# Kernel tuning notes

Hardware: AMD Instinct MI355X
Metric: run time of the kernel (lower is better)

The kernel has to match this reference:

```python
import jax, jax.numpy as jnp
import numpy as np

D_K = 64  # key/query head dim used for the 1/sqrt(d_k) scale


def setup_inputs() -> dict:
    key0 = jax.random.key(0)
    kk, kq, kv = jax.random.split(key0, 3)
    B, H, S, DK, DV = 2, 16, 2048, 64, 64
    return {
        "key": jax.random.normal(kk, (B, H, S, DK), dtype=jnp.float32),
        "query": jax.random.normal(kq, (B, H, S, DK), dtype=jnp.float32),
        "value": jax.random.normal(kv, (B, H, S, DV), dtype=jnp.float32),
    }


def reference(key, query, value):
    # scaled dot-product attention per head: [B,H,S,S]
    scores = jnp.einsum("bhqd,bhkd->bhqk", query, key) / jnp.sqrt(jnp.asarray(D_K, query.dtype))
    attn = jax.nn.softmax(scores, axis=-1)
    out = jnp.einsum("bhqk,bhkv->bhqv", attn, value)  # [B,H,S,d_v]
    B, H, S, DV = out.shape
    # faithful to the torch .view: raw reshape (no head transpose)
    return out.reshape(B, S, H * DV)
```

## Files before the change

kernel.cpp:

```cpp
#include <hip/hip_runtime.h>

#define S_LEN 2048
#define DHEAD 64
#define BHEADS 32
#define BM 128
#define BN 64
#define NTILES (S_LEN / BN)
#define HEAD_ELEMS (S_LEN * DHEAD)
#define TENS_ELEMS (BHEADS * HEAD_ELEMS)

typedef _Float16 half8_t __attribute__((ext_vector_type(8)));
typedef _Float16 half4_t __attribute__((ext_vector_type(4)));
typedef _Float16 half2_t __attribute__((ext_vector_type(2)));
typedef float float4_t __attribute__((ext_vector_type(4)));

#define SC_LOG2E 0.18033688011112042f

__device__ __forceinline__ void async_cp16(const void* g, void* l) {
    __builtin_amdgcn_global_load_lds(
        (const __attribute__((address_space(1))) unsigned int*)g,
        (__attribute__((address_space(3))) unsigned int*)l, 16, 0, 0);
}

__global__ void prep_kernel(const float* __restrict__ K,
                            const float* __restrict__ V,
                            _Float16* __restrict__ K16,
                            _Float16* __restrict__ VT) {
    __shared__ _Float16 tile[64][72];
    const int bh = blockIdx.x >> 5;
    const int s0 = (blockIdx.x & 31) * 64;
    const int tid = threadIdx.x;

    const float4* ks = (const float4*)(K + (bh * S_LEN + s0) * DHEAD);
    half4_t* kd = (half4_t*)(K16 + (bh * S_LEN + s0) * DHEAD);
    const float4* vs = (const float4*)(V + (bh * S_LEN + s0) * DHEAD);
#pragma unroll
    for (int it = 0; it < 4; ++it) {
        int i = it * 256 + tid;
        float4 kv = ks[i];
        half4_t h = {(_Float16)(kv.x * SC_LOG2E), (_Float16)(kv.y * SC_LOG2E),
                     (_Float16)(kv.z * SC_LOG2E), (_Float16)(kv.w * SC_LOG2E)};
        kd[i] = h;
        float4 vv = vs[i];
        int r = i >> 4, c4 = (i & 15) * 4;
        half4_t hv = {(_Float16)vv.x, (_Float16)vv.y, (_Float16)vv.z, (_Float16)vv.w};
        *(half4_t*)&tile[r][c4] = hv;
    }
    __syncthreads();
    _Float16* vd = VT + bh * HEAD_ELEMS + s0;
#pragma unroll
    for (int it = 0; it < 2; ++it) {
        int c = it * 256 + tid;
        int vrow = c >> 3, p0 = (c & 7) * 8;
        half8_t h;
#pragma unroll
        for (int j = 0; j < 8; ++j) {
            int p = p0 + j, pc = p >> 2;
            int key = ((pc >> 3) << 5) + ((pc & 1) << 4) + (((pc >> 1) & 3) << 2) + (p & 3);
            h[j] = tile[key][vrow];
        }
        *(half8_t*)(vd + vrow * S_LEN + p0) = h;
    }
}


__global__ __launch_bounds__(256) void attn_kernel(
    const float* __restrict__ Qf,
    const _Float16* __restrict__ K16,
    const _Float16* __restrict__ VT16,
    float* __restrict__ out) {
    __shared__ __align__(16) _Float16 sQ[BM * DHEAD];
    __shared__ __align__(16) _Float16 sK[2][BN * DHEAD];
    __shared__ __align__(16) _Float16 sVT[2][BN * DHEAD];

    const int tid = threadIdx.x;
    const int wave = tid >> 6;
    const int lane = tid & 63;
    const int ln15 = lane & 15;
    const int g = lane >> 4;

    const int bh = blockIdx.x >> 4;
    const int q0 = (blockIdx.x & 15) * BM;

    const float* Qg = Qf + (bh * S_LEN + q0) * DHEAD;
    const _Float16* Kg = K16 + bh * HEAD_ELEMS;
    const _Float16* Vg = VT16 + bh * HEAD_ELEMS;

    const int c0 = tid, c1 = tid + 256;
    const int r0 = c0 >> 3, r1 = c1 >> 3;
    const int sl0 = (c0 - r0) & 7, sl1 = (c1 - r1) & 7;
    const _Float16* ksrc0 = Kg + r0 * DHEAD + sl0 * 8;
    const _Float16* ksrc1 = Kg + r1 * DHEAD + sl1 * 8;
    const _Float16* vsrc0 = Vg + r0 * S_LEN + sl0 * 8;
    const _Float16* vsrc1 = Vg + r1 * S_LEN + sl1 * 8;
    _Float16* kd0[2] = {sK[0] + c0 * 8, sK[1] + c0 * 8};
    _Float16* kd1[2] = {sK[0] + c1 * 8, sK[1] + c1 * 8};
    _Float16* vd0[2] = {sVT[0] + c0 * 8, sVT[1] + c0 * 8};
    _Float16* vd1[2] = {sVT[0] + c1 * 8, sVT[1] + c1 * 8};

    async_cp16(ksrc0, kd0[0]);
    async_cp16(ksrc1, kd1[0]);
    async_cp16(vsrc0, vd0[0]);
    async_cp16(vsrc1, vd1[0]);

#pragma unroll
    for (int tt = 0; tt < 4; ++tt) {
        int c = tid + tt * 256;
        int row = c >> 3;
        int lsl = (c - row) & 7;
        const float4* src = (const float4*)(Qg + row * DHEAD + lsl * 8);
        float4 v0 = src[0];
        float4 v1 = src[1];
        half8_t h = {(_Float16)v0.x, (_Float16)v0.y, (_Float16)v0.z, (_Float16)v0.w,
                     (_Float16)v1.x, (_Float16)v1.y, (_Float16)v1.z, (_Float16)v1.w};
        *(half8_t*)((char*)sQ + c * 16) = h;
    }
    __syncthreads();

    half8_t qf[2][2];
#pragma unroll
    for (int nq = 0; nq < 2; ++nq) {
        int qrow = wave * 32 + nq * 16 + ln15;
        const char* qb = (const char*)sQ + qrow * 128;
        qf[nq][0] = *(const half8_t*)(qb + ((g * 16 + qrow * 16) & 127));
        qf[nq][1] = *(const half8_t*)(qb + ((64 + g * 16 + qrow * 16) & 127));
    }

    float lsum[2] = {0.f, 0.f};
    float4_t o[2][4];
#pragma unroll
    for (int nq = 0; nq < 2; ++nq)
#pragma unroll
        for (int vt = 0; vt < 4; ++vt) o[nq][vt] = (float4_t){0.f, 0.f, 0.f, 0.f};

    for (int t = 0; t < NTILES; ++t) {
        const int cur = t & 1;
        if (t + 1 < NTILES) {
            const _Float16* kb0 = ksrc0 + (t + 1) * (BN * DHEAD);
            const _Float16* kb1 = ksrc1 + (t + 1) * (BN * DHEAD);
            const _Float16* vb0 = vsrc0 + (t + 1) * BN;
            const _Float16* vb1 = vsrc1 + (t + 1) * BN;
            async_cp16(kb0, kd0[cur ^ 1]);
            async_cp16(kb1, kd1[cur ^ 1]);
            async_cp16(vb0, vd0[cur ^ 1]);
            async_cp16(vb1, vd1[cur ^ 1]);
        }

        half4_t pb[2][4];
        const char* kb = (const char*)sK[cur];
#pragma unroll
        for (int mt = 0; mt < 4; ++mt) {
            int row = mt * 16 + ln15;
            const char* rb = kb + row * 128;
            half8_t a0 = *(const half8_t*)(rb + ((g * 16 + row * 16) & 127));
            half8_t a1 = *(const half8_t*)(rb + ((64 + g * 16 + row * 16) & 127));
#pragma unroll
            for (int nq = 0; nq < 2; ++nq) {
                float4_t c0 = (float4_t){0.f, 0.f, 0.f, 0.f};
                c0 = __builtin_amdgcn_mfma_f32_16x16x32_f16(a0, qf[nq][0], c0, 0, 0, 0);
                c0 = __builtin_amdgcn_mfma_f32_16x16x32_f16(a1, qf[nq][1], c0, 0, 0, 0);
                float p0 = __builtin_amdgcn_exp2f(c0[0]);
                float p1 = __builtin_amdgcn_exp2f(c0[1]);
                float p2 = __builtin_amdgcn_exp2f(c0[2]);
                float p3 = __builtin_amdgcn_exp2f(c0[3]);
                lsum[nq] += (p0 + p1) + (p2 + p3);
                half2_t lo = __builtin_bit_cast(half2_t, __builtin_amdgcn_cvt_pkrtz(p0, p1));
                half2_t hi = __builtin_bit_cast(half2_t, __builtin_amdgcn_cvt_pkrtz(p2, p3));
                pb[nq][mt] = (half4_t){lo[0], lo[1], hi[0], hi[1]};
            }
        }

        const char* vb = (const char*)sVT[cur];
#pragma unroll
        for (int vt = 0; vt < 4; ++vt) {
            int vrow = vt * 16 + ln15;
            const char* rb = vb + vrow * 128;
#pragma unroll
            for (int ktp = 0; ktp < 2; ++ktp) {
                half8_t va = *(const half8_t*)(rb + ((ktp * 64 + g * 16 + vrow * 16) & 127));
                half4_t alo = __builtin_shufflevector(va, va, 0, 1, 2, 3);
                half4_t ahi = __builtin_shufflevector(va, va, 4, 5, 6, 7);
#pragma unroll
                for (int nq = 0; nq < 2; ++nq) {
                    o[nq][vt] = __builtin_amdgcn_mfma_f32_16x16x16f16(alo, pb[nq][2 * ktp], o[nq][vt], 0, 0, 0);
                    o[nq][vt] = __builtin_amdgcn_mfma_f32_16x16x16f16(ahi, pb[nq][2 * ktp + 1], o[nq][vt], 0, 0, 0);
                }
            }
        }
        __syncthreads();
    }

#pragma unroll
    for (int nq = 0; nq < 2; ++nq) {
        float l = lsum[nq];
        l += __shfl_xor(l, 16, 64);
        l += __shfl_xor(l, 32, 64);
        float inv_l = 1.0f / l;
        int qg = q0 + wave * 32 + nq * 16 + ln15;
        float* og = out + (bh * S_LEN + qg) * DHEAD;
#pragma unroll
        for (int vt = 0; vt < 4; ++vt) {
            float4_t vals;
            vals[0] = o[nq][vt][0] * inv_l;
            vals[1] = o[nq][vt][1] * inv_l;
            vals[2] = o[nq][vt][2] * inv_l;
            vals[3] = o[nq][vt][3] * inv_l;
            *(float4_t*)(og + vt * 16 + g * 4) = vals;
        }
    }
}


extern "C" void kernel_launch(void* const* d_in, const int* in_sizes, int n_in,
                              void* d_out, int out_size, void* d_ws, size_t ws_size,
                              hipStream_t stream) {
    const float* Kf = (const float*)d_in[0];
    const float* Qf = (const float*)d_in[1];
    const float* Vf = (const float*)d_in[2];
    float* out = (float*)d_out;

    _Float16* K16 = (_Float16*)d_ws;
    _Float16* VT16 = K16 + TENS_ELEMS;

    prep_kernel<<<BHEADS * (S_LEN / 64), 256, 0, stream>>>(Kf, Vf, K16, VT16);
    attn_kernel<<<BHEADS * (S_LEN / BM), 256, 0, stream>>>(Qf, K16, VT16, out);
}
```

Measured before the change: 142.3 us.

## Pre-swizzle K/V into MFMA fragment layout and load straight to registers

The prep kernel now writes K and V in a per-tile fragment order that matches the MFMA operand layout. The attention kernel drops shared memory and barriers: each wave reads K/V fragments directly from global memory into double-buffered registers and loads Q from global itself. This removes LDS traffic and the block-wide sync, and lets waves run independently. In exchange, each wave re-reads K/V from global or L2 with no sharing through LDS, and register pressure goes up.

Result: faster. 137.8 us (-3.2%).

```diff
diff --git a/kernel.cpp b/kernel.cpp
--- a/kernel.cpp
+++ b/kernel.cpp
@@ -3,11 +3,10 @@
 #define S_LEN 2048
 #define DHEAD 64
 #define BHEADS 32
-#define BM 128
-#define BN 64
-#define NTILES (S_LEN / BN)
+#define NTILES 32
 #define HEAD_ELEMS (S_LEN * DHEAD)
 #define TENS_ELEMS (BHEADS * HEAD_ELEMS)
+#define TILE_HALVES 4096
 
 typedef _Float16 half8_t __attribute__((ext_vector_type(8)));
 typedef _Float16 half4_t __attribute__((ext_vector_type(4)));
@@ -16,114 +15,99 @@
 
 #define SC_LOG2E 0.18033688011112042f
 
-__device__ __forceinline__ void async_cp16(const void* g, void* l) {
-    __builtin_amdgcn_global_load_lds(
-        (const __attribute__((address_space(1))) unsigned int*)g,
-        (__attribute__((address_space(3))) unsigned int*)l, 16, 0, 0);
-}
-
-__global__ void prep_kernel(const float* __restrict__ K,
-                            const float* __restrict__ V,
-                            _Float16* __restrict__ K16,
-                            _Float16* __restrict__ VT) {
+
+__global__ __launch_bounds__(256) void prep_kernel(const float* __restrict__ K,
+                                                   const float* __restrict__ V,
+                                                   _Float16* __restrict__ Kf,
+                                                   _Float16* __restrict__ Vf) {
     __shared__ _Float16 tile[64][72];
     const int bh = blockIdx.x >> 5;
-    const int s0 = (blockIdx.x & 31) * 64;
+    const int t = blockIdx.x & 31;
     const int tid = threadIdx.x;
 
-    const float4* ks = (const float4*)(K + (bh * S_LEN + s0) * DHEAD);
-    half4_t* kd = (half4_t*)(K16 + (bh * S_LEN + s0) * DHEAD);
-    const float4* vs = (const float4*)(V + (bh * S_LEN + s0) * DHEAD);
+    const float* Ksrc = K + (bh * S_LEN + t * 64) * DHEAD;
+    const float4* vs = (const float4*)(V + (bh * S_LEN + t * 64) * DHEAD);
 #pragma unroll
     for (int it = 0; it < 4; ++it) {
         int i = it * 256 + tid;
-        float4 kv = ks[i];
-        half4_t h = {(_Float16)(kv.x * SC_LOG2E), (_Float16)(kv.y * SC_LOG2E),
-                     (_Float16)(kv.z * SC_LOG2E), (_Float16)(kv.w * SC_LOG2E)};
-        kd[i] = h;
         float4 vv = vs[i];
         int r = i >> 4, c4 = (i & 15) * 4;
         half4_t hv = {(_Float16)vv.x, (_Float16)vv.y, (_Float16)vv.z, (_Float16)vv.w};
         *(half4_t*)&tile[r][c4] = hv;
     }
-    __syncthreads();
-    _Float16* vd = VT + bh * HEAD_ELEMS + s0;
+
+    _Float16* kd = Kf + (bh * NTILES + t) * TILE_HALVES;
 #pragma unroll
     for (int it = 0; it < 2; ++it) {
         int c = it * 256 + tid;
-        int vrow = c >> 3, p0 = (c & 7) * 8;
+        int f = c >> 6, lane = c & 63;
+        int row = (f >> 1) * 16 + (lane & 15);
+        int d0 = (f & 1) * 32 + (lane >> 4) * 8;
+        const float4* s = (const float4*)(Ksrc + row * DHEAD + d0);
+        float4 a = s[0], b = s[1];
+        half8_t h = {(_Float16)(a.x * SC_LOG2E), (_Float16)(a.y * SC_LOG2E),
+                     (_Float16)(a.z * SC_LOG2E), (_Float16)(a.w * SC_LOG2E),
+                     (_Float16)(b.x * SC_LOG2E), (_Float16)(b.y * SC_LOG2E),
+                     (_Float16)(b.z * SC_LOG2E), (_Float16)(b.w * SC_LOG2E)};
+        *(half8_t*)(kd + c * 8) = h;
+    }
+    __syncthreads();
+
+    _Float16* vd = Vf + (bh * NTILES + t) * TILE_HALVES;
+#pragma unroll
+    for (int it = 0; it < 2; ++it) {
+        int c = it * 256 + tid;
+        int fv = c >> 6, lane = c & 63;
+        int vt = fv >> 1, ktp = fv & 1;
+        int v = vt * 16 + (lane & 15);
+        int g = lane >> 4;
         half8_t h;
 #pragma unroll
         for (int j = 0; j < 8; ++j) {
-            int p = p0 + j, pc = p >> 2;
-            int key = ((pc >> 3) << 5) + ((pc & 1) << 4) + (((pc >> 1) & 3) << 2) + (p & 3);
-            h[j] = tile[key][vrow];
-        }
-        *(half8_t*)(vd + vrow * S_LEN + p0) = h;
+            int key = ktp * 32 + (j >> 2) * 16 + g * 4 + (j & 3);
+            h[j] = tile[key][v];
+        }
+        *(half8_t*)(vd + c * 8) = h;
     }
 }
 
 
-__global__ __launch_bounds__(256) void attn_kernel(
+__global__ __launch_bounds__(256, 2) void attn_kernel(
     const float* __restrict__ Qf,
-    const _Float16* __restrict__ K16,
-    const _Float16* __restrict__ VT16,
+    const _Float16* __restrict__ Kf,
+    const _Float16* __restrict__ Vf,
     float* __restrict__ out) {
-    __shared__ __align__(16) _Float16 sQ[BM * DHEAD];
-    __shared__ __align__(16) _Float16 sK[2][BN * DHEAD];
-    __shared__ __align__(16) _Float16 sVT[2][BN * DHEAD];
-
     const int tid = threadIdx.x;
-    const int wave = tid >> 6;
+    const int wid = tid >> 6;
     const int lane = tid & 63;
     const int ln15 = lane & 15;
     const int g = lane >> 4;
 
-    const int bh = blockIdx.x >> 4;
-    const int q0 = (blockIdx.x & 15) * BM;
+    const int gwave = blockIdx.x * 4 + wid;
+    const int bh = gwave >> 6;
+    const int q0 = (gwave & 63) * 32;
 
     const float* Qg = Qf + (bh * S_LEN + q0) * DHEAD;
-    const _Float16* Kg = K16 + bh * HEAD_ELEMS;
-    const _Float16* Vg = VT16 + bh * HEAD_ELEMS;
-
-    const int c0 = tid, c1 = tid + 256;
-    const int r0 = c0 >> 3, r1 = c1 >> 3;
-    const int sl0 = (c0 - r0) & 7, sl1 = (c1 - r1) & 7;
-    const _Float16* ksrc0 = Kg + r0 * DHEAD + sl0 * 8;
-    const _Float16* ksrc1 = Kg + r1 * DHEAD + sl1 * 8;
-    const _Float16* vsrc0 = Vg + r0 * S_LEN + sl0 * 8;
-    const _Float16* vsrc1 = Vg + r1 * S_LEN + sl1 * 8;
-    _Float16* kd0[2] = {sK[0] + c0 * 8, sK[1] + c0 * 8};
-    _Float16* kd1[2] = {sK[0] + c1 * 8, sK[1] + c1 * 8};
-    _Float16* vd0[2] = {sVT[0] + c0 * 8, sVT[1] + c0 * 8};
-    _Float16* vd1[2] = {sVT[0] + c1 * 8, sVT[1] + c1 * 8};
-
-    async_cp16(ksrc0, kd0[0]);
-    async_cp16(ksrc1, kd1[0]);
-    async_cp16(vsrc0, vd0[0]);
-    async_cp16(vsrc1, vd1[0]);
-
-#pragma unroll
-    for (int tt = 0; tt < 4; ++tt) {
-        int c = tid + tt * 256;
-        int row = c >> 3;
-        int lsl = (c - row) & 7;
-        const float4* src = (const float4*)(Qg + row * DHEAD + lsl * 8);
-        float4 v0 = src[0];
-        float4 v1 = src[1];
-        half8_t h = {(_Float16)v0.x, (_Float16)v0.y, (_Float16)v0.z, (_Float16)v0.w,
-                     (_Float16)v1.x, (_Float16)v1.y, (_Float16)v1.z, (_Float16)v1.w};
-        *(half8_t*)((char*)sQ + c * 16) = h;
-    }
-    __syncthreads();
-
     half8_t qf[2][2];
 #pragma unroll
-    for (int nq = 0; nq < 2; ++nq) {
-        int qrow = wave * 32 + nq * 16 + ln15;
-        const char* qb = (const char*)sQ + qrow * 128;
-        qf[nq][0] = *(const half8_t*)(qb + ((g * 16 + qrow * 16) & 127));
-        qf[nq][1] = *(const half8_t*)(qb + ((64 + g * 16 + qrow * 16) & 127));
+    for (int nq = 0; nq < 2; ++nq)
+#pragma unroll
+        for (int kh = 0; kh < 2; ++kh) {
+            const float4* qs = (const float4*)(Qg + (nq * 16 + ln15) * DHEAD + kh * 32 + g * 8);
+            float4 a = qs[0], b = qs[1];
+            qf[nq][kh] = (half8_t){(_Float16)a.x, (_Float16)a.y, (_Float16)a.z, (_Float16)a.w,
+                                   (_Float16)b.x, (_Float16)b.y, (_Float16)b.z, (_Float16)b.w};
+        }
+
+    const _Float16* kb = Kf + bh * (NTILES * TILE_HALVES);
+    const _Float16* vb = Vf + bh * (NTILES * TILE_HALVES);
+    const int lo = lane * 8;
+
+    half8_t kf[2][8], vf[2][8];
+#pragma unroll
+    for (int f = 0; f < 8; ++f) {
+        kf[0][f] = *(const half8_t*)(kb + f * 512 + lo);
+        vf[0][f] = *(const half8_t*)(vb + f * 512 + lo);
     }
 
     float lsum[2] = {0.f, 0.f};
@@ -133,27 +117,23 @@
 #pragma unroll
         for (int vt = 0; vt < 4; ++vt) o[nq][vt] = (float4_t){0.f, 0.f, 0.f, 0.f};
 
+#pragma unroll 2
     for (int t = 0; t < NTILES; ++t) {
         const int cur = t & 1;
-        if (t + 1 < NTILES) {
-            const _Float16* kb0 = ksrc0 + (t + 1) * (BN * DHEAD);
-            const _Float16* kb1 = ksrc1 + (t + 1) * (BN * DHEAD);
-            const _Float16* vb0 = vsrc0 + (t + 1) * BN;
-            const _Float16* vb1 = vsrc1 + (t + 1) * BN;
-            async_cp16(kb0, kd0[cur ^ 1]);
-            async_cp16(kb1, kd1[cur ^ 1]);
-            async_cp16(vb0, vd0[cur ^ 1]);
-            async_cp16(vb1, vd1[cur ^ 1]);
+        const int tn = (t + 1 < NTILES) ? t + 1 : t;
+        const _Float16* kbn = kb + tn * TILE_HALVES;
+        const _Float16* vbn = vb + tn * TILE_HALVES;
+#pragma unroll
+        for (int f = 0; f < 8; ++f) {
+            kf[cur ^ 1][f] = *(const half8_t*)(kbn + f * 512 + lo);
+            vf[cur ^ 1][f] = *(const half8_t*)(vbn + f * 512 + lo);
         }
 
         half4_t pb[2][4];
-        const char* kb = (const char*)sK[cur];
 #pragma unroll
         for (int mt = 0; mt < 4; ++mt) {
-            int row = mt * 16 + ln15;
-            const char* rb = kb + row * 128;
-            half8_t a0 = *(const half8_t*)(rb + ((g * 16 + row * 16) & 127));
-            half8_t a1 = *(const half8_t*)(rb + ((64 + g * 16 + row * 16) & 127));
+            half8_t a0 = kf[cur][mt * 2];
+            half8_t a1 = kf[cur][mt * 2 + 1];
 #pragma unroll
             for (int nq = 0; nq < 2; ++nq) {
                 float4_t c0 = (float4_t){0.f, 0.f, 0.f, 0.f};
@@ -164,20 +144,17 @@
                 float p2 = __builtin_amdgcn_exp2f(c0[2]);
                 float p3 = __builtin_amdgcn_exp2f(c0[3]);
                 lsum[nq] += (p0 + p1) + (p2 + p3);
-                half2_t lo = __builtin_bit_cast(half2_t, __builtin_amdgcn_cvt_pkrtz(p0, p1));
-                half2_t hi = __builtin_bit_cast(half2_t, __builtin_amdgcn_cvt_pkrtz(p2, p3));
-                pb[nq][mt] = (half4_t){lo[0], lo[1], hi[0], hi[1]};
+                half2_t plo = __builtin_bit_cast(half2_t, __builtin_amdgcn_cvt_pkrtz(p0, p1));
+                half2_t phi = __builtin_bit_cast(half2_t, __builtin_amdgcn_cvt_pkrtz(p2, p3));
+                pb[nq][mt] = (half4_t){plo[0], plo[1], phi[0], phi[1]};
             }
         }
 
-        const char* vb = (const char*)sVT[cur];
 #pragma unroll
         for (int vt = 0; vt < 4; ++vt) {
-            int vrow = vt * 16 + ln15;
-            const char* rb = vb + vrow * 128;
 #pragma unroll
             for (int ktp = 0; ktp < 2; ++ktp) {
-                half8_t va = *(const half8_t*)(rb + ((ktp * 64 + g * 16 + vrow * 16) & 127));
+                half8_t va = vf[cur][vt * 2 + ktp];
                 half4_t alo = __builtin_shufflevector(va, va, 0, 1, 2, 3);
                 half4_t ahi = __builtin_shufflevector(va, va, 4, 5, 6, 7);
 #pragma unroll
@@ -187,7 +164,6 @@
                 }
             }
         }
-        __syncthreads();
     }
 
 #pragma unroll
@@ -196,7 +172,7 @@
         l += __shfl_xor(l, 16, 64);
         l += __shfl_xor(l, 32, 64);
         float inv_l = 1.0f / l;
-        int qg = q0 + wave * 32 + nq * 16 + ln15;
+        int qg = q0 + nq * 16 + ln15;
         float* og = out + (bh * S_LEN + qg) * DHEAD;
 #pragma unroll
         for (int vt = 0; vt < 4; ++vt) {
@@ -214,14 +190,14 @@
 extern "C" void kernel_launch(void* const* d_in, const int* in_sizes, int n_in,
                               void* d_out, int out_size, void* d_ws, size_t ws_size,
                               hipStream_t stream) {
-    const float* Kf = (const float*)d_in[0];
-    const float* Qf = (const float*)d_in[1];
-    const float* Vf = (const float*)d_in[2];
+    const float* Kin = (const float*)d_in[0];
+    const float* Qin = (const float*)d_in[1];
+    const float* Vin = (const float*)d_in[2];
     float* out = (float*)d_out;
 
-    _Float16* K16 = (_Float16*)d_ws;
-    _Float16* VT16 = K16 + TENS_ELEMS;
-
-    prep_kernel<<<BHEADS * (S_LEN / 64), 256, 0, stream>>>(Kf, Vf, K16, VT16);
-    attn_kernel<<<BHEADS * (S_LEN / BM), 256, 0, stream>>>(Qf, K16, VT16, out);
+    _Float16* Kf = (_Float16*)d_ws;
+    _Float16* Vf = Kf + TENS_ELEMS;
+
+    prep_kernel<<<BHEADS * NTILES, 256, 0, stream>>>(Kin, Vin, Kf, Vf);
+    attn_kernel<<<BHEADS * 64 / 4, 256, 0, stream>>>(Qin, Kf, Vf, out);
 }
```
